# Performance work log

Hardware: AMD Instinct MI355X
Metric: run time of the kernel (lower is better)

Reference implementation:

```python
import jax, jax.numpy as jnp
import numpy as np

B, S, IN, H, D, M, OUT = 1, 4096, 2048, 2048, 1024, 65536, 2048
TOP_K = 3
EPS = 1e-12  # F.normalize eps


def setup_inputs() -> dict:
    key = jax.random.key(0)
    ks = jax.random.split(key, 13)
    def g(k, shape, scale):
        return jax.random.normal(k, shape, dtype=jnp.float32) * scale
    return {
        "x": g(ks[0], (B, S, IN), 1.0),
        "W1": g(ks[1], (IN, H), (1.0 / IN) ** 0.5),
        "b1": g(ks[2], (H,), 0.01),
        "W2": g(ks[3], (H, H), (1.0 / H) ** 0.5),
        "b2": g(ks[4], (H,), 0.01),
        "Wq": g(ks[5], (H, D), (1.0 / H) ** 0.5),
        "bq": g(ks[6], (D,), 0.01),
        "Wout": g(ks[7], (H + D, OUT), (1.0 / (H + D)) ** 0.5),
        "bout": g(ks[8], (OUT,), 0.01),
        "keys": g(ks[9], (M, D), 1.0),
        "values": g(ks[10], (M, D), 1.0),
        "importance": jax.random.uniform(ks[11], (M,), dtype=jnp.float32),
    }


def _l2norm(v):
    n = jnp.sqrt(jnp.sum(v * v, axis=-1, keepdims=True))
    return v / jnp.maximum(n, EPS)


def reference(x, W1, b1, W2, b2, Wq, bq, Wout, bout, keys, values, importance):
    # controller: Linear -> ReLU -> Linear over flattened tokens
    h = jnp.maximum(x.reshape(-1, IN) @ W1 + b1, 0.0) @ W2 + b2  # [B*S, H]
    h = h.reshape(B, S, H)
    last_hidden = h[:, -1, :]                                    # [B=1, H]
    # query generation + cosine similarity against memory keys
    q = last_hidden @ Wq + bq                                    # [1, D]
    qn = _l2norm(q)
    kn = _l2norm(keys)                                           # [M, D]
    sims = (qn @ kn.T)[0]                                        # [M]
    weighted = sims * importance                                 # [M]
    top_vals, top_idx = jax.lax.top_k(weighted, TOP_K)
    attn = jax.nn.softmax(top_vals)                              # [K]
    retrieved = attn @ values[top_idx]                           # [D]
    combined = jnp.concatenate([last_hidden, retrieved[None, :]], axis=-1)  # [1, H+D]
    out = combined @ Wout + bout                                 # [1, OUT]
    return out
```

## Files before the change

kernel.cpp:

```cpp
#include <hip/hip_runtime.h>

#define FEPS 1e-12f

__device__ __forceinline__ void top3_insert(float val, int idx,
                                            float& v0, float& v1, float& v2,
                                            int& i0, int& i1, int& i2) {
    if (val > v0)      { v2 = v1; i2 = i1; v1 = v0; i1 = i0; v0 = val; i0 = idx; }
    else if (val > v1) { v2 = v1; i2 = i1; v1 = val; i1 = idx; }
    else if (val > v2) { v2 = val; i2 = idx; }
}

template<int RELU>
__global__ void gemv_atomic4(const float* __restrict__ v,
                             const float* __restrict__ W,
                             const float* __restrict__ bias,
                             float* __restrict__ out,
                             int C, int chunk) {
    int j = (blockIdx.x * 256 + threadIdx.x) * 4;
    int i0 = blockIdx.y * chunk;
    float4 acc = make_float4(0.f, 0.f, 0.f, 0.f);
    for (int i = i0; i < i0 + chunk; ++i) {
        float vi = v[i];
        if (RELU) vi = fmaxf(vi, 0.f);
        float4 w = *(const float4*)(W + (size_t)i * C + j);
        acc.x += vi * w.x; acc.y += vi * w.y;
        acc.z += vi * w.z; acc.w += vi * w.w;
    }
    if (blockIdx.y == 0) {
        float4 b = *(const float4*)(bias + j);
        acc.x += b.x; acc.y += b.y; acc.z += b.z; acc.w += b.w;
    }
    atomicAdd(&out[j + 0], acc.x);
    atomicAdd(&out[j + 1], acc.y);
    atomicAdd(&out[j + 2], acc.z);
    atomicAdd(&out[j + 3], acc.w);
}

__global__ void sims_top3_fused(const float* __restrict__ q,
                                const float* __restrict__ keys,
                                const float* __restrict__ imp,
                                const float* __restrict__ values,
                                float* __restrict__ cand_val,
                                int* __restrict__ cand_idx,
                                unsigned* __restrict__ ctr,
                                float* __restrict__ retr,
                                float* __restrict__ out) {
    __shared__ float qs[1024];
    __shared__ float wv[4 * 3];
    __shared__ int   wi[4 * 3];
    __shared__ float s_red[4];
    __shared__ float s_attn[3];
    __shared__ int   s_idx[3];
    __shared__ int   s_last;
    int t = threadIdx.x;
    #pragma unroll
    for (int p = 0; p < 4; ++p) qs[t + 256 * p] = q[t + 256 * p];
    __syncthreads();
    int wave = t >> 6, lane = t & 63;
    const float4* q4 = (const float4*)qs;
    float4 qv[4];
    #pragma unroll
    for (int p = 0; p < 4; ++p) qv[p] = q4[lane + 64 * p];

    float v0 = -INFINITY, v1 = -INFINITY, v2 = -INFINITY;
    int   i0 = -1, i1 = -1, i2 = -1;
    int mbase = blockIdx.x * 32 + wave * 8;
    for (int r = 0; r < 8; ++r) {
        int m = mbase + r;
        const float4* krow = (const float4*)(keys + (size_t)m * 1024);
        float dot = 0.f, sq = 0.f;
        #pragma unroll
        for (int p = 0; p < 4; ++p) {
            float4 k = krow[lane + 64 * p];
            dot += k.x * qv[p].x + k.y * qv[p].y + k.z * qv[p].z + k.w * qv[p].w;
            sq  += k.x * k.x + k.y * k.y + k.z * k.z + k.w * k.w;
        }
        #pragma unroll
        for (int off = 32; off; off >>= 1) {
            dot += __shfl_down(dot, off);
            sq  += __shfl_down(sq, off);
        }
        if (lane == 0) {
            float val = dot * imp[m] / fmaxf(sqrtf(sq), FEPS);
            top3_insert(val, m, v0, v1, v2, i0, i1, i2);
        }
    }
    if (lane == 0) {
        wv[wave * 3 + 0] = v0; wv[wave * 3 + 1] = v1; wv[wave * 3 + 2] = v2;
        wi[wave * 3 + 0] = i0; wi[wave * 3 + 1] = i1; wi[wave * 3 + 2] = i2;
    }
    __syncthreads();
    if (t == 0) {
        float a0 = -INFINITY, a1 = -INFINITY, a2 = -INFINITY;
        int   b0 = -1, b1 = -1, b2 = -1;
        for (int e = 0; e < 12; ++e)
            top3_insert(wv[e], wi[e], a0, a1, a2, b0, b1, b2);
        int base = blockIdx.x * 3;
        __hip_atomic_store(&cand_val[base + 0], a0, __ATOMIC_RELAXED, __HIP_MEMORY_SCOPE_AGENT);
        __hip_atomic_store(&cand_val[base + 1], a1, __ATOMIC_RELAXED, __HIP_MEMORY_SCOPE_AGENT);
        __hip_atomic_store(&cand_val[base + 2], a2, __ATOMIC_RELAXED, __HIP_MEMORY_SCOPE_AGENT);
        __hip_atomic_store(&cand_idx[base + 0], b0, __ATOMIC_RELAXED, __HIP_MEMORY_SCOPE_AGENT);
        __hip_atomic_store(&cand_idx[base + 1], b1, __ATOMIC_RELAXED, __HIP_MEMORY_SCOPE_AGENT);
        __hip_atomic_store(&cand_idx[base + 2], b2, __ATOMIC_RELAXED, __HIP_MEMORY_SCOPE_AGENT);
        __threadfence();
        unsigned tk = __hip_atomic_fetch_add(ctr, 1u, __ATOMIC_ACQ_REL, __HIP_MEMORY_SCOPE_AGENT);
        s_last = (tk == gridDim.x - 1) ? 1 : 0;
    }
    __syncthreads();
    if (!s_last) return;

    __threadfence();
    float pq = 0.f;
    #pragma unroll
    for (int p = 0; p < 4; ++p) { float x = qs[t + 256 * p]; pq = fmaf(x, x, pq); }
    #pragma unroll
    for (int off = 32; off; off >>= 1) pq += __shfl_down(pq, off);

    float c0 = -INFINITY, c1 = -INFINITY, c2 = -INFINITY;
    int   d0 = -1, d1 = -1, d2 = -1;
    #pragma unroll
    for (int kk = 0; kk < 24; ++kk) {
        int c = t + (kk << 8);
        float val = __hip_atomic_load(&cand_val[c], __ATOMIC_RELAXED, __HIP_MEMORY_SCOPE_AGENT);
        int   idx = __hip_atomic_load(&cand_idx[c], __ATOMIC_RELAXED, __HIP_MEMORY_SCOPE_AGENT);
        top3_insert(val, idx, c0, c1, c2, d0, d1, d2);
    }
    #pragma unroll
    for (int off = 32; off; off >>= 1) {
        float u0 = __shfl_down(c0, off), u1 = __shfl_down(c1, off), u2 = __shfl_down(c2, off);
        int   j0 = __shfl_down(d0, off), j1 = __shfl_down(d1, off), j2 = __shfl_down(d2, off);
        top3_insert(u0, j0, c0, c1, c2, d0, d1, d2);
        top3_insert(u1, j1, c0, c1, c2, d0, d1, d2);
        top3_insert(u2, j2, c0, c1, c2, d0, d1, d2);
    }
    if (lane == 0) {
        wv[wave * 3 + 0] = c0; wv[wave * 3 + 1] = c1; wv[wave * 3 + 2] = c2;
        wi[wave * 3 + 0] = d0; wi[wave * 3 + 1] = d1; wi[wave * 3 + 2] = d2;
        s_red[wave] = pq;
    }
    __syncthreads();
    if (t == 0) {
        float a0 = -INFINITY, a1 = -INFINITY, a2 = -INFINITY;
        int   b0 = -1, b1 = -1, b2 = -1;
        for (int e = 0; e < 12; ++e)
            top3_insert(wv[e], wi[e], a0, a1, a2, b0, b1, b2);
        float qden = fmaxf(sqrtf(s_red[0] + s_red[1] + s_red[2] + s_red[3]), FEPS);
        float tv0 = a0 / qden, tv1 = a1 / qden, tv2 = a2 / qden;
        float mx = fmaxf(tv0, fmaxf(tv1, tv2));
        float e0 = expf(tv0 - mx), e1 = expf(tv1 - mx), e2 = expf(tv2 - mx);
        float sum = e0 + e1 + e2;
        s_attn[0] = e0 / sum; s_attn[1] = e1 / sum; s_attn[2] = e2 / sum;
        s_idx[0] = b0; s_idx[1] = b1; s_idx[2] = b2;
    }
    __syncthreads();

    #pragma unroll
    for (int p = 0; p < 4; ++p) {
        int col = t + 256 * p;
        float r = s_attn[0] * values[(size_t)s_idx[0] * 1024 + col]
                + s_attn[1] * values[(size_t)s_idx[1] * 1024 + col]
                + s_attn[2] * values[(size_t)s_idx[2] * 1024 + col];
        retr[col] = r;
    }
    #pragma unroll
    for (int p = 0; p < 8; ++p) out[t + 256 * p] = 0.0f;
}

extern "C" void kernel_launch(void* const* d_in, const int* in_sizes, int n_in,
                              void* d_out, int out_size, void* d_ws, size_t ws_size,
                              hipStream_t stream) {
    const float* x      = (const float*)d_in[0];
    const float* W1     = (const float*)d_in[1];
    const float* b1     = (const float*)d_in[2];
    const float* W2     = (const float*)d_in[3];
    const float* b2     = (const float*)d_in[4];
    const float* Wq     = (const float*)d_in[5];
    const float* bq     = (const float*)d_in[6];
    const float* Wout   = (const float*)d_in[7];
    const float* bout   = (const float*)d_in[8];
    const float* keys   = (const float*)d_in[9];
    const float* values = (const float*)d_in[10];
    const float* imp    = (const float*)d_in[11];
    float* out = (float*)d_out;
    float* ws  = (float*)d_ws;

    float*    h1       = ws;
    float*    comb     = ws + 2048;
    float*    retr     = ws + 4096;
    float*    q        = ws + 5120;
    unsigned* ctr      = (unsigned*)(ws + 6144);
    float*    cand_val = ws + 6160;
    int*      cand_idx = (int*)(ws + 12304);

    const float* xlast = x + (size_t)(4096 - 1) * 2048;

    hipMemsetAsync(d_ws, 0, 6160 * sizeof(float), stream);

    gemv_atomic4<0><<<dim3(2, 128), 256, 0, stream>>>(xlast, W1, b1, h1, 2048, 16);
    gemv_atomic4<1><<<dim3(2, 128), 256, 0, stream>>>(h1, W2, b2, comb, 2048, 16);
    gemv_atomic4<0><<<dim3(1, 128), 256, 0, stream>>>(comb, Wq, bq, q, 1024, 16);
    sims_top3_fused<<<2048, 256, 0, stream>>>(q, keys, imp, values,
                                              cand_val, cand_idx, ctr, retr, out);
    gemv_atomic4<0><<<dim3(2, 128), 256, 0, stream>>>(comb, Wout, bout, out, 2048, 24);
}
```

Measured before the change: 706.1 us.

## Compute key similarities thread-per-row with single-wave blocks and staggered chunk order

The similarity/top-3 kernel moves from a wave cooperating on each key row (with shuffle reductions per row) to each thread computing a full 1024-wide row on its own, in 64-thread blocks. Each block starts at a rotated 128-byte chunk offset to spread memory channel traffic. The final merge, softmax and gather use wave shuffles and float4 accesses instead of shared memory and block barriers. The trade-off is uncoalesced 4KB-strided loads across lanes and far fewer resident waves, which may hurt bandwidth on the 256MB key scan.

```diff
diff --git a/kernel.cpp b/kernel.cpp
--- a/kernel.cpp
+++ b/kernel.cpp
@@ -36,134 +36,134 @@
     atomicAdd(&out[j + 3], acc.w);
 }
 
-__global__ void sims_top3_fused(const float* __restrict__ q,
-                                const float* __restrict__ keys,
-                                const float* __restrict__ imp,
-                                const float* __restrict__ values,
-                                float* __restrict__ cand_val,
-                                int* __restrict__ cand_idx,
-                                unsigned* __restrict__ ctr,
-                                float* __restrict__ retr,
-                                float* __restrict__ out) {
+__global__ __launch_bounds__(64)
+void sims_top3_rows(const float* __restrict__ q,
+                    const float* __restrict__ keys,
+                    const float* __restrict__ imp,
+                    const float* __restrict__ values,
+                    float* __restrict__ cand_val,
+                    int* __restrict__ cand_idx,
+                    unsigned* __restrict__ ctr,
+                    float* __restrict__ retr,
+                    float* __restrict__ out) {
     __shared__ float qs[1024];
-    __shared__ float wv[4 * 3];
-    __shared__ int   wi[4 * 3];
-    __shared__ float s_red[4];
-    __shared__ float s_attn[3];
-    __shared__ int   s_idx[3];
-    __shared__ int   s_last;
     int t = threadIdx.x;
     #pragma unroll
-    for (int p = 0; p < 4; ++p) qs[t + 256 * p] = q[t + 256 * p];
+    for (int p = 0; p < 4; ++p)
+        *(float4*)(qs + (t + 64 * p) * 4) = *(const float4*)(q + (t + 64 * p) * 4);
     __syncthreads();
-    int wave = t >> 6, lane = t & 63;
-    const float4* q4 = (const float4*)qs;
-    float4 qv[4];
-    #pragma unroll
-    for (int p = 0; p < 4; ++p) qv[p] = q4[lane + 64 * p];
-
-    float v0 = -INFINITY, v1 = -INFINITY, v2 = -INFINITY;
-    int   i0 = -1, i1 = -1, i2 = -1;
-    int mbase = blockIdx.x * 32 + wave * 8;
-    for (int r = 0; r < 8; ++r) {
-        int m = mbase + r;
-        const float4* krow = (const float4*)(keys + (size_t)m * 1024);
-        float dot = 0.f, sq = 0.f;
+
+    int m = blockIdx.x * 64 + t;
+    const float* krow = keys + (size_t)m * 1024;
+    int c0 = (blockIdx.x * 5) & 31;
+    float dot0 = 0.f, dot1 = 0.f, sq0 = 0.f, sq1 = 0.f;
+    #pragma unroll 2
+    for (int s = 0; s < 32; ++s) {
+        int c = (c0 + s) & 31;
+        const float4* kc = (const float4*)(krow + c * 32);
+        const float4* qc = (const float4*)(qs + c * 32);
+        float4 k[8], qv[8];
         #pragma unroll
-        for (int p = 0; p < 4; ++p) {
-            float4 k = krow[lane + 64 * p];
-            dot += k.x * qv[p].x + k.y * qv[p].y + k.z * qv[p].z + k.w * qv[p].w;
-            sq  += k.x * k.x + k.y * k.y + k.z * k.z + k.w * k.w;
+        for (int j = 0; j < 8; ++j) k[j] = kc[j];
+        #pragma unroll
+        for (int j = 0; j < 8; ++j) qv[j] = qc[j];
+        #pragma unroll
+        for (int j = 0; j < 8; j += 2) {
+            dot0 += k[j].x * qv[j].x + k[j].y * qv[j].y
+                  + k[j].z * qv[j].z + k[j].w * qv[j].w;
+            sq0  += k[j].x * k[j].x + k[j].y * k[j].y
+                  + k[j].z * k[j].z + k[j].w * k[j].w;
+            dot1 += k[j+1].x * qv[j+1].x + k[j+1].y * qv[j+1].y
+                  + k[j+1].z * qv[j+1].z + k[j+1].w * qv[j+1].w;
+            sq1  += k[j+1].x * k[j+1].x + k[j+1].y * k[j+1].y
+                  + k[j+1].z * k[j+1].z + k[j+1].w * k[j+1].w;
         }
-        #pragma unroll
-        for (int off = 32; off; off >>= 1) {
-            dot += __shfl_down(dot, off);
-            sq  += __shfl_down(sq, off);
-        }
-        if (lane == 0) {
-            float val = dot * imp[m] / fmaxf(sqrtf(sq), FEPS);
-            top3_insert(val, m, v0, v1, v2, i0, i1, i2);
-        }
-    }
-    if (lane == 0) {
-        wv[wave * 3 + 0] = v0; wv[wave * 3 + 1] = v1; wv[wave * 3 + 2] = v2;
-        wi[wave * 3 + 0] = i0; wi[wave * 3 + 1] = i1; wi[wave * 3 + 2] = i2;
-    }
-    __syncthreads();
+    }
+    float val = (dot0 + dot1) * imp[m] / fmaxf(sqrtf(sq0 + sq1), FEPS);
+
+    float v0 = val, v1 = -INFINITY, v2 = -INFINITY;
+    int   i0 = m,   i1 = -1, i2 = -1;
+    #pragma unroll
+    for (int off = 32; off; off >>= 1) {
+        float u0 = __shfl_down(v0, off), u1 = __shfl_down(v1, off), u2 = __shfl_down(v2, off);
+        int   j0 = __shfl_down(i0, off), j1 = __shfl_down(i1, off), j2 = __shfl_down(i2, off);
+        top3_insert(u0, j0, v0, v1, v2, i0, i1, i2);
+        top3_insert(u1, j1, v0, v1, v2, i0, i1, i2);
+        top3_insert(u2, j2, v0, v1, v2, i0, i1, i2);
+    }
+
+    int last = 0;
     if (t == 0) {
-        float a0 = -INFINITY, a1 = -INFINITY, a2 = -INFINITY;
-        int   b0 = -1, b1 = -1, b2 = -1;
-        for (int e = 0; e < 12; ++e)
-            top3_insert(wv[e], wi[e], a0, a1, a2, b0, b1, b2);
         int base = blockIdx.x * 3;
-        __hip_atomic_store(&cand_val[base + 0], a0, __ATOMIC_RELAXED, __HIP_MEMORY_SCOPE_AGENT);
-        __hip_atomic_store(&cand_val[base + 1], a1, __ATOMIC_RELAXED, __HIP_MEMORY_SCOPE_AGENT);
-        __hip_atomic_store(&cand_val[base + 2], a2, __ATOMIC_RELAXED, __HIP_MEMORY_SCOPE_AGENT);
-        __hip_atomic_store(&cand_idx[base + 0], b0, __ATOMIC_RELAXED, __HIP_MEMORY_SCOPE_AGENT);
-        __hip_atomic_store(&cand_idx[base + 1], b1, __ATOMIC_RELAXED, __HIP_MEMORY_SCOPE_AGENT);
-        __hip_atomic_store(&cand_idx[base + 2], b2, __ATOMIC_RELAXED, __HIP_MEMORY_SCOPE_AGENT);
+        __hip_atomic_store(&cand_val[base + 0], v0, __ATOMIC_RELAXED, __HIP_MEMORY_SCOPE_AGENT);
+        __hip_atomic_store(&cand_val[base + 1], v1, __ATOMIC_RELAXED, __HIP_MEMORY_SCOPE_AGENT);
+        __hip_atomic_store(&cand_val[base + 2], v2, __ATOMIC_RELAXED, __HIP_MEMORY_SCOPE_AGENT);
+        __hip_atomic_store(&cand_idx[base + 0], i0, __ATOMIC_RELAXED, __HIP_MEMORY_SCOPE_AGENT);
+        __hip_atomic_store(&cand_idx[base + 1], i1, __ATOMIC_RELAXED, __HIP_MEMORY_SCOPE_AGENT);
+        __hip_atomic_store(&cand_idx[base + 2], i2, __ATOMIC_RELAXED, __HIP_MEMORY_SCOPE_AGENT);
         __threadfence();
         unsigned tk = __hip_atomic_fetch_add(ctr, 1u, __ATOMIC_ACQ_REL, __HIP_MEMORY_SCOPE_AGENT);
-        s_last = (tk == gridDim.x - 1) ? 1 : 0;
-    }
-    __syncthreads();
-    if (!s_last) return;
+        last = (tk == gridDim.x - 1) ? 1 : 0;
+    }
+    last = __shfl(last, 0);
+    if (!last) return;
 
     __threadfence();
     float pq = 0.f;
     #pragma unroll
-    for (int p = 0; p < 4; ++p) { float x = qs[t + 256 * p]; pq = fmaf(x, x, pq); }
+    for (int p = 0; p < 16; ++p) { float x = qs[t + 64 * p]; pq = fmaf(x, x, pq); }
     #pragma unroll
     for (int off = 32; off; off >>= 1) pq += __shfl_down(pq, off);
 
-    float c0 = -INFINITY, c1 = -INFINITY, c2 = -INFINITY;
+    float c0v = -INFINITY, c1v = -INFINITY, c2v = -INFINITY;
     int   d0 = -1, d1 = -1, d2 = -1;
-    #pragma unroll
-    for (int kk = 0; kk < 24; ++kk) {
-        int c = t + (kk << 8);
-        float val = __hip_atomic_load(&cand_val[c], __ATOMIC_RELAXED, __HIP_MEMORY_SCOPE_AGENT);
-        int   idx = __hip_atomic_load(&cand_idx[c], __ATOMIC_RELAXED, __HIP_MEMORY_SCOPE_AGENT);
-        top3_insert(val, idx, c0, c1, c2, d0, d1, d2);
+    for (int kk = 0; kk < 48; ++kk) {
+        int c = t + (kk << 6);
+        float cv = __hip_atomic_load(&cand_val[c], __ATOMIC_RELAXED, __HIP_MEMORY_SCOPE_AGENT);
+        int   ci = __hip_atomic_load(&cand_idx[c], __ATOMIC_RELAXED, __HIP_MEMORY_SCOPE_AGENT);
+        top3_insert(cv, ci, c0v, c1v, c2v, d0, d1, d2);
     }
     #pragma unroll
     for (int off = 32; off; off >>= 1) {
-        float u0 = __shfl_down(c0, off), u1 = __shfl_down(c1, off), u2 = __shfl_down(c2, off);
-        int   j0 = __shfl_down(d0, off), j1 = __shfl_down(d1, off), j2 = __shfl_down(d2, off);
-        top3_insert(u0, j0, c0, c1, c2, d0, d1, d2);
-        top3_insert(u1, j1, c0, c1, c2, d0, d1, d2);
-        top3_insert(u2, j2, c0, c1, c2, d0, d1, d2);
-    }
-    if (lane == 0) {
-        wv[wave * 3 + 0] = c0; wv[wave * 3 + 1] = c1; wv[wave * 3 + 2] = c2;
-        wi[wave * 3 + 0] = d0; wi[wave * 3 + 1] = d1; wi[wave * 3 + 2] = d2;
-        s_red[wave] = pq;
-    }
-    __syncthreads();
+        float u0 = __shfl_down(c0v, off), u1 = __shfl_down(c1v, off), u2 = __shfl_down(c2v, off);
+        int   j0 = __shfl_down(d0, off),  j1 = __shfl_down(d1, off),  j2 = __shfl_down(d2, off);
+        top3_insert(u0, j0, c0v, c1v, c2v, d0, d1, d2);
+        top3_insert(u1, j1, c0v, c1v, c2v, d0, d1, d2);
+        top3_insert(u2, j2, c0v, c1v, c2v, d0, d1, d2);
+    }
+
+    float attn0 = 0.f, attn1 = 0.f, attn2 = 0.f;
+    int   id0 = 0, id1 = 0, id2 = 0;
     if (t == 0) {
-        float a0 = -INFINITY, a1 = -INFINITY, a2 = -INFINITY;
-        int   b0 = -1, b1 = -1, b2 = -1;
-        for (int e = 0; e < 12; ++e)
-            top3_insert(wv[e], wi[e], a0, a1, a2, b0, b1, b2);
-        float qden = fmaxf(sqrtf(s_red[0] + s_red[1] + s_red[2] + s_red[3]), FEPS);
-        float tv0 = a0 / qden, tv1 = a1 / qden, tv2 = a2 / qden;
+        float qden = fmaxf(sqrtf(pq), FEPS);
+        float tv0 = c0v / qden, tv1 = c1v / qden, tv2 = c2v / qden;
         float mx = fmaxf(tv0, fmaxf(tv1, tv2));
         float e0 = expf(tv0 - mx), e1 = expf(tv1 - mx), e2 = expf(tv2 - mx);
         float sum = e0 + e1 + e2;
-        s_attn[0] = e0 / sum; s_attn[1] = e1 / sum; s_attn[2] = e2 / sum;
-        s_idx[0] = b0; s_idx[1] = b1; s_idx[2] = b2;
-    }
-    __syncthreads();
-
+        attn0 = e0 / sum; attn1 = e1 / sum; attn2 = e2 / sum;
+        id0 = d0; id1 = d1; id2 = d2;
+    }
+    attn0 = __shfl(attn0, 0); attn1 = __shfl(attn1, 0); attn2 = __shfl(attn2, 0);
+    id0 = __shfl(id0, 0); id1 = __shfl(id1, 0); id2 = __shfl(id2, 0);
+
+    const float4* V0 = (const float4*)(values + (size_t)id0 * 1024);
+    const float4* V1 = (const float4*)(values + (size_t)id1 * 1024);
+    const float4* V2 = (const float4*)(values + (size_t)id2 * 1024);
+    float4* retr4 = (float4*)retr;
     #pragma unroll
     for (int p = 0; p < 4; ++p) {
-        int col = t + 256 * p;
-        float r = s_attn[0] * values[(size_t)s_idx[0] * 1024 + col]
-                + s_attn[1] * values[(size_t)s_idx[1] * 1024 + col]
-                + s_attn[2] * values[(size_t)s_idx[2] * 1024 + col];
-        retr[col] = r;
-    }
-    #pragma unroll
-    for (int p = 0; p < 8; ++p) out[t + 256 * p] = 0.0f;
+        int c4 = t + 64 * p;
+        float4 a = V0[c4], b = V1[c4], c = V2[c4], r;
+        r.x = attn0 * a.x + attn1 * b.x + attn2 * c.x;
+        r.y = attn0 * a.y + attn1 * b.y + attn2 * c.y;
+        r.z = attn0 * a.z + attn1 * b.z + attn2 * c.z;
+        r.w = attn0 * a.w + attn1 * b.w + attn2 * c.w;
+        retr4[c4] = r;
+    }
+    float4* out4 = (float4*)out;
+    float4 z = make_float4(0.f, 0.f, 0.f, 0.f);
+    #pragma unroll
+    for (int p = 0; p < 8; ++p) out4[t + 64 * p] = z;
 }
 
 extern "C" void kernel_launch(void* const* d_in, const int* in_sizes, int n_in,
@@ -190,7 +190,7 @@
     float*    q        = ws + 5120;
     unsigned* ctr      = (unsigned*)(ws + 6144);
     float*    cand_val = ws + 6160;
-    int*      cand_idx = (int*)(ws + 12304);
+    int*      cand_idx = (int*)(ws + 9232);
 
     const float* xlast = x + (size_t)(4096 - 1) * 2048;
 
@@ -199,7 +199,7 @@
     gemv_atomic4<0><<<dim3(2, 128), 256, 0, stream>>>(xlast, W1, b1, h1, 2048, 16);
     gemv_atomic4<1><<<dim3(2, 128), 256, 0, stream>>>(h1, W2, b2, comb, 2048, 16);
     gemv_atomic4<0><<<dim3(1, 128), 256, 0, stream>>>(comb, Wq, bq, q, 1024, 16);
-    sims_top3_fused<<<2048, 256, 0, stream>>>(q, keys, imp, values,
-                                              cand_val, cand_idx, ctr, retr, out);
+    sims_top3_rows<<<1024, 64, 0, stream>>>(q, keys, imp, values,
+                                            cand_val, cand_idx, ctr, retr, out);
     gemv_atomic4<0><<<dim3(2, 128), 256, 0, stream>>>(comb, Wout, bout, out, 2048, 24);
 }
```

New measurement: 698.9 us. About the same (-1.0%).
